# Kernel tuning notes

Measured on AMD Instinct MI355X. Metric: run time of the kernel, lower is better.

## Reference

```python
import jax, jax.numpy as jnp
import numpy as np

N_EMBEDS = 1024
N_HEADS = 16
EPS = 1e-3


def layer_norm(x, gamma, beta):
    mean = jnp.mean(x, axis=-1, keepdims=True)
    var = jnp.mean((x - mean) ** 2, axis=-1, keepdims=True)
    return gamma * (x - mean) / jnp.sqrt(var + EPS) + beta


def setup_inputs() -> dict:
    key = jax.random.key(0)
    ks = jax.random.split(key, 8)
    B, T, C = 4, 2048, N_EMBEDS
    s = 1.0 / np.sqrt(C)
    return {
        "x": jax.random.normal(ks[0], (B, T, C), dtype=jnp.float32),
        "w_qkv": jax.random.normal(ks[1], (C, 3 * C), dtype=jnp.float32) * s,
        "w_proj": jax.random.normal(ks[2], (C, C), dtype=jnp.float32) * s,
        "b_proj": jnp.zeros((C,), dtype=jnp.float32),
        "w1": jax.random.normal(ks[3], (C, 4 * C), dtype=jnp.float32) * s,
        "b1": jnp.zeros((4 * C,), dtype=jnp.float32),
        "w2": jax.random.normal(ks[4], (4 * C, C), dtype=jnp.float32) * (0.5 / np.sqrt(C)),
        "b2": jnp.zeros((C,), dtype=jnp.float32),
        "gamma1": jnp.ones((C,), dtype=jnp.float32),
        "beta1": jnp.zeros((C,), dtype=jnp.float32),
        "gamma2": jnp.ones((C,), dtype=jnp.float32),
        "beta2": jnp.zeros((C,), dtype=jnp.float32),
    }


def reference(x, w_qkv, w_proj, b_proj, w1, b1, w2, b2, gamma1, beta1, gamma2, beta2):
    B, T, C = x.shape
    H = N_HEADS
    D = C // H
    scale = D ** -0.5

    # --- attention sub-layer (pre-LN) ---
    h = layer_norm(x, gamma1, beta1)
    qkv = h @ w_qkv                      # [B,T,3C]
    q, k, v = jnp.split(qkv, 3, axis=-1)
    q = q.reshape(B, T, H, D).transpose(0, 2, 1, 3)  # [B,H,T,D]
    k = k.reshape(B, T, H, D).transpose(0, 2, 1, 3)
    v = v.reshape(B, T, H, D).transpose(0, 2, 1, 3)
    att = jnp.einsum('bhqd,bhkd->bhqk', q, k) * scale
    causal = jnp.tril(jnp.ones((T, T), dtype=bool))
    att = jnp.where(causal[None, None], att, jnp.float32(-1e9))
    att = jax.nn.softmax(att, axis=-1)
    out = jnp.einsum('bhqk,bhkd->bhqd', att, v)
    out = out.transpose(0, 2, 1, 3).reshape(B, T, C)
    x = x + out @ w_proj + b_proj

    # --- FFN sub-layer (pre-LN, erf-GELU) ---
    h = layer_norm(x, gamma2, beta2)
    h = jax.nn.gelu(h @ w1 + b1, approximate=False)
    x = x + h @ w2 + b2
    return x
```

## Files before the change

### kernel.cpp

```cpp
#include <hip/hip_runtime.h>
#include <hip/hip_bf16.h>
#include <cstdint>
#include <cstddef>

#define B_ 4
#define T_ 2048
#define C_ 1024
#define H_ 16
#define D_ 64
#define M_ (B_*T_)

using bf16_t = __hip_bfloat16;
typedef __bf16 v8bf __attribute__((ext_vector_type(8)));
typedef float  v4f  __attribute__((ext_vector_type(4)));
typedef float  f32x16 __attribute__((ext_vector_type(16)));

#define QSCALE (0.125f * 1.44269504088896340736f)

static __device__ __forceinline__ bf16_t f2bf(float v){ return __float2bfloat16(v); }

static __device__ __forceinline__ void glds16(const bf16_t* g, bf16_t* l){
  __builtin_amdgcn_global_load_lds((__attribute__((address_space(1))) void*)g,
                                   (__attribute__((address_space(3))) void*)l, 16, 0, 0);
}

static __device__ __forceinline__ uint32_t cvt_pk_bf16(float lo, float hi){
  uint32_t w;
  asm("v_cvt_pk_bf16_f32 %0, %1, %2" : "=v"(w) : "v"(lo), "v"(hi));
  return w;
}

__global__ void k_transpose_cast(const float* __restrict__ in, bf16_t* __restrict__ out,
                                 int K, int N){
  __shared__ float tile[32][33];
  int k0 = blockIdx.y*32, n0 = blockIdx.x*32;
  int tx = threadIdx.x, ty = threadIdx.y;
  #pragma unroll
  for(int j=0;j<32;j+=8) tile[ty+j][tx] = in[(size_t)(k0+ty+j)*N + n0+tx];
  __syncthreads();
  #pragma unroll
  for(int j=0;j<32;j+=8) out[(size_t)(n0+ty+j)*K + k0+tx] = f2bf(tile[tx][ty+j]);
}

__global__ __launch_bounds__(256) void k_layernorm(const float* __restrict__ x,
                                                   const float* __restrict__ gamma,
                                                   const float* __restrict__ beta,
                                                   bf16_t* __restrict__ out){
  int row = blockIdx.x;
  int tid = threadIdx.x;
  const float4 v = reinterpret_cast<const float4*>(x + (size_t)row*C_)[tid];
  float s  = v.x+v.y+v.z+v.w;
  float ss = v.x*v.x+v.y*v.y+v.z*v.z+v.w*v.w;
  #pragma unroll
  for(int m=1;m<64;m<<=1){ s += __shfl_xor(s,m); ss += __shfl_xor(ss,m); }
  __shared__ float sbuf[4], ssbuf[4];
  int wid = tid>>6, lane = tid&63;
  if(lane==0){ sbuf[wid]=s; ssbuf[wid]=ss; }
  __syncthreads();
  s  = sbuf[0]+sbuf[1]+sbuf[2]+sbuf[3];
  ss = ssbuf[0]+ssbuf[1]+ssbuf[2]+ssbuf[3];
  float mean = s * (1.0f/C_);
  float var  = ss * (1.0f/C_) - mean*mean;
  float rstd = rsqrtf(var + 1e-3f);
  const float4 g = reinterpret_cast<const float4*>(gamma)[tid];
  const float4 b = reinterpret_cast<const float4*>(beta)[tid];
  union { ushort4 u; bf16_t h[4]; } pk;
  pk.h[0] = f2bf(g.x*(v.x-mean)*rstd + b.x);
  pk.h[1] = f2bf(g.y*(v.y-mean)*rstd + b.y);
  pk.h[2] = f2bf(g.z*(v.z-mean)*rstd + b.z);
  pk.h[3] = f2bf(g.w*(v.w-mean)*rstd + b.w);
  *reinterpret_cast<ushort4*>(out + (size_t)row*C_ + tid*4) = pk.u;
}

template<int MODE>
__global__ __launch_bounds__(512, 4)
void k_gemm(const bf16_t* __restrict__ A, const bf16_t* __restrict__ Bt,
            const float* __restrict__ bias, const float* resid,
            void* out0, void* out1, void* out2,
            int N, int K, int gx)
{
  __shared__ __align__(16) bf16_t As[2][256*32];
  __shared__ __align__(16) bf16_t Bs[2][128*32];
  const int tid = threadIdx.x, lane = tid & 63, w = tid >> 6;
  const int wm = w >> 1, wn = w & 1;

  const int nwg = gx * 32;
  const int orig = blockIdx.y * gx + blockIdx.x;
  const int swz = (orig & 7) * (nwg >> 3) + (orig >> 3);
  const int ct = swz % gx, rt = swz / gx;
  const int row0 = rt * 256, col0 = ct * 128;

  const int sswz  = ((lane & 3) ^ ((lane >> 3) & 3)) * 8;
  const int srowA = w * 32 + (lane >> 2);
  const int srowB = w * 16 + (lane >> 2);
  const bf16_t* Ag = A  + (size_t)(row0 + srowA) * K + sswz;
  const bf16_t* Bg = Bt + (size_t)(col0 + srowB) * K + sswz;

  const int rdswz = (((lane >> 4) ^ (((lane & 15) >> 1) & 3))) * 8;

  v4f acc[4][4] = {};
  const int NT = K >> 5;

  auto stage = [&](int tt, int bb){
    const size_t ko = (size_t)tt * 32;
    glds16(Ag + ko,                 &As[bb][(w*32     )*32]);
    glds16(Ag + (size_t)16*K + ko,  &As[bb][(w*32 + 16)*32]);
    glds16(Bg + ko,                 &Bs[bb][(w*16     )*32]);
  };

  stage(0, 0);
  for (int t = 0; t < NT; ++t) {
    const int b = t & 1;
    if (t + 1 < NT) {
      stage(t + 1, b ^ 1);
      asm volatile("s_waitcnt vmcnt(3)" ::: "memory");
    } else {
      asm volatile("s_waitcnt vmcnt(0)" ::: "memory");
    }
    __builtin_amdgcn_s_barrier();
    __builtin_amdgcn_sched_barrier(0);
    const bf16_t* Ab = &As[b][0];
    const bf16_t* Bb = &Bs[b][0];
    v8bf af[4], bfv[4];
    #pragma unroll
    for (int m = 0; m < 4; ++m) {
      const int r = wm*64 + m*16 + (lane & 15);
      af[m] = *reinterpret_cast<const v8bf*>(Ab + r*32 + rdswz);
    }
    #pragma unroll
    for (int n = 0; n < 4; ++n) {
      const int r = wn*64 + n*16 + (lane & 15);
      bfv[n] = *reinterpret_cast<const v8bf*>(Bb + r*32 + rdswz);
    }
    __builtin_amdgcn_s_setprio(1);
    #pragma unroll
    for (int m = 0; m < 4; ++m)
      #pragma unroll
      for (int n = 0; n < 4; ++n)
        acc[m][n] = __builtin_amdgcn_mfma_f32_16x16x32_bf16(af[m], bfv[n], acc[m][n], 0,0,0);
    __builtin_amdgcn_s_setprio(0);
    __builtin_amdgcn_sched_barrier(0);
    __builtin_amdgcn_s_barrier();
  }

  #pragma unroll
  for (int mf = 0; mf < 4; ++mf) {
    const int rbase = row0 + wm*64 + mf*16 + (lane>>4)*4;
    #pragma unroll
    for (int nf = 0; nf < 4; ++nf) {
      const int c = col0 + wn*64 + nf*16 + (lane&15);
      #pragma unroll
      for (int i = 0; i < 4; ++i) {
        const int rr = rbase + i;
        float v = acc[mf][nf][i];
        if constexpr(MODE==0){
          const int sec = c >> 10, cc = c & 1023;
          const int h = cc >> 6, d = cc & 63;
          const int b = rr >> 11, t = rr & 2047;
          if(sec==0)      ((bf16_t*)out0)[((size_t)(b*H_ + h)*T_ + t)*D_ + d] = f2bf(v * QSCALE);
          else if(sec==1) ((bf16_t*)out1)[((size_t)(b*H_ + h)*T_ + t)*D_ + d] = f2bf(v);
          else            ((bf16_t*)out2)[((size_t)(b*H_ + h)*D_ + d)*T_ + t] = f2bf(v);
        } else if constexpr(MODE==1){
          ((float*)out0)[(size_t)rr*N + c] = v + bias[c] + resid[(size_t)rr*N + c];
        } else if constexpr(MODE==2){
          float o = v + bias[c];
          o = 0.5f*o*(1.0f + erff(o*0.70710678118f));
          ((bf16_t*)out0)[(size_t)rr*N + c] = f2bf(o);
        } else {
          ((float*)out0)[(size_t)rr*N + c] = v + bias[c] + resid[(size_t)rr*N + c];
        }
      }
    }
  }
}

__global__ __launch_bounds__(256)
void k_attn(const bf16_t* __restrict__ Q, const bf16_t* __restrict__ Kg,
            const bf16_t* __restrict__ Vt, bf16_t* __restrict__ O)
{
  __shared__ __align__(16) bf16_t Ks [64][72];
  __shared__ __align__(16) bf16_t Vts[64][72];
  __shared__ __align__(16) bf16_t Os [128][72];
  const int bh = blockIdx.y;
  const int pair = blockIdx.x;
  const int tid = threadIdx.x, lane = tid & 63, w = tid >> 6;
  const int ql = lane & 31, hi = lane >> 5;
  const int srow = tid >> 2;
  const int scol = (tid & 3) * 16;
  const bf16_t* Kgp = Kg + ((size_t)bh*T_ + srow)*D_ + scol;
  const bf16_t* Vtp = Vt + ((size_t)bh*D_ + srow)*T_ + scol;
  const int b = bh >> 4, h = bh & 15;

  for(int half=0; half<2; ++half){
    const int qt = half ? pair : (15 - pair);
    const int qbase = qt*128 + w*32;
    const int q = qbase + ql;

    v8bf qf[4];
    {
      const bf16_t* Qb = Q + ((size_t)bh*T_ + q)*D_ + hi*8;
      #pragma unroll
      for(int ds=0; ds<4; ds++)
        qf[ds] = *reinterpret_cast<const v8bf*>(Qb + ds*16);
    }

    f32x16 accO[2] = {};
    float mrun = -1e30f, lrun = 0.0f;
    const int NT = (qt + 1) * 2;

    v8bf kr0 = *reinterpret_cast<const v8bf*>(Kgp);
    v8bf kr1 = *reinterpret_cast<const v8bf*>(Kgp + 8);
    v8bf vr0 = *reinterpret_cast<const v8bf*>(Vtp);
    v8bf vr1 = *reinterpret_cast<const v8bf*>(Vtp + 8);

    for(int t=0; t<NT; t++){
      const int kv0 = t*64;
      *reinterpret_cast<v8bf*>(&Ks [srow][scol  ]) = kr0;
      *reinterpret_cast<v8bf*>(&Ks [srow][scol+8]) = kr1;
      *reinterpret_cast<v8bf*>(&Vts[srow][scol  ]) = vr0;
      *reinterpret_cast<v8bf*>(&Vts[srow][scol+8]) = vr1;
      __syncthreads();
      if(t+1 < NT){
        const size_t kn = (size_t)(kv0 + 64);
        kr0 = *reinterpret_cast<const v8bf*>(Kgp + kn*D_);
        kr1 = *reinterpret_cast<const v8bf*>(Kgp + kn*D_ + 8);
        vr0 = *reinterpret_cast<const v8bf*>(Vtp + kn);
        vr1 = *reinterpret_cast<const v8bf*>(Vtp + kn + 8);
      }

      if(kv0 <= qbase + 31){
        f32x16 sT[2] = {};
        #pragma unroll
        for(int kvh=0; kvh<2; kvh++)
          #pragma unroll
          for(int ds=0; ds<4; ds++){
            v8bf kf = *reinterpret_cast<const v8bf*>(&Ks[kvh*32 + ql][ds*16 + hi*8]);
            sT[kvh] = __builtin_amdgcn_mfma_f32_32x32x16_bf16(kf, qf[ds], sT[kvh], 0,0,0);
          }

        if(kv0 + 63 > qbase){
          const int qrel = q - kv0 - hi*4;
          #pragma unroll
          for(int kvh=0; kvh<2; kvh++)
            #pragma unroll
            for(int r=0; r<16; r++){
              const int c = kvh*32 + (r&3) + 8*(r>>2);
              if(c > qrel) sT[kvh][r] = -1e30f;
            }
        }

        float pm = sT[0][0];
        #pragma unroll
        for(int r=1; r<16; r++) pm = fmaxf(pm, sT[0][r]);
        #pragma unroll
        for(int r=0; r<16; r++) pm = fmaxf(pm, sT[1][r]);
        pm = fmaxf(pm, __shfl_xor(pm, 32));

        if(__any(pm - mrun > 8.0f)){
          const float mnew = fmaxf(mrun, pm);
          const float corr = __builtin_amdgcn_exp2f(mrun - mnew);
          mrun = mnew;
          lrun *= corr;
          #pragma unroll
          for(int dh=0; dh<2; dh++)
            #pragma unroll
            for(int r=0; r<16; r++) accO[dh][r] *= corr;
        }

        float rs = 0.0f;
        #pragma unroll
        for(int kvh=0; kvh<2; kvh++)
          #pragma unroll
          for(int r=0; r<16; r++){
            float p = __builtin_amdgcn_exp2f(sT[kvh][r] - mrun);
            sT[kvh][r] = p;
            rs += p;
          }
        rs += __shfl_xor(rs, 32);
        lrun += rs;

        v8bf pfrag[4];
        #pragma unroll
        for(int s4=0; s4<4; s4++){
          const int kvh = s4>>1, bb = (s4&1)*8;
          uint32_t wa = cvt_pk_bf16(sT[kvh][bb+0], sT[kvh][bb+1]);
          uint32_t wb = cvt_pk_bf16(sT[kvh][bb+2], sT[kvh][bb+3]);
          uint32_t wc = cvt_pk_bf16(sT[kvh][bb+4], sT[kvh][bb+5]);
          uint32_t wd = cvt_pk_bf16(sT[kvh][bb+6], sT[kvh][bb+7]);
          uint32_t xwa = (uint32_t)__shfl_xor((int)wa, 32);
          uint32_t xwb = (uint32_t)__shfl_xor((int)wb, 32);
          uint32_t xwc = (uint32_t)__shfl_xor((int)wc, 32);
          uint32_t xwd = (uint32_t)__shfl_xor((int)wd, 32);
          union { uint32_t u[4]; v8bf v; } pk;
          pk.u[0] = hi ? xwc : wa;
          pk.u[1] = hi ? xwd : wb;
          pk.u[2] = hi ? wc  : xwa;
          pk.u[3] = hi ? wd  : xwb;
          pfrag[s4] = pk.v;
        }

        #pragma unroll
        for(int dh=0; dh<2; dh++)
          #pragma unroll
          for(int s4=0; s4<4; s4++){
            v8bf vf = *reinterpret_cast<const v8bf*>(&Vts[dh*32 + ql][s4*16 + hi*8]);
            accO[dh] = __builtin_amdgcn_mfma_f32_32x32x16_bf16(vf, pfrag[s4], accO[dh], 0,0,0);
          }
      }
      __syncthreads();
    }

    const float inv = 1.0f / lrun;
    #pragma unroll
    for(int dh=0; dh<2; dh++)
      #pragma unroll
      for(int rg=0; rg<4; rg++){
        uint32_t lo_ = cvt_pk_bf16(accO[dh][rg*4+0]*inv, accO[dh][rg*4+1]*inv);
        uint32_t hi_ = cvt_pk_bf16(accO[dh][rg*4+2]*inv, accO[dh][rg*4+3]*inv);
        uint2 w2; w2.x = lo_; w2.y = hi_;
        *reinterpret_cast<uint2*>(&Os[w*32 + ql][dh*32 + rg*8 + hi*4]) = w2;
      }
    __syncthreads();
    const int orow = tid >> 1, ocol = (tid & 1) * 32;
    bf16_t* Og = O + ((size_t)(b*T_ + qt*128 + orow))*C_ + h*64 + ocol;
    #pragma unroll
    for(int j=0;j<4;j++)
      *reinterpret_cast<v8bf*>(Og + j*8) = *reinterpret_cast<const v8bf*>(&Os[orow][ocol + j*8]);
    __syncthreads();
  }
}

extern "C" void kernel_launch(void* const* d_in, const int* in_sizes, int n_in,
                              void* d_out, int out_size, void* d_ws, size_t ws_size,
                              hipStream_t stream) {
  const float* x      = (const float*)d_in[0];
  const float* w_qkv  = (const float*)d_in[1];
  const float* w_proj = (const float*)d_in[2];
  const float* b_proj = (const float*)d_in[3];
  const float* w1     = (const float*)d_in[4];
  const float* b1     = (const float*)d_in[5];
  const float* w2     = (const float*)d_in[6];
  const float* b2     = (const float*)d_in[7];
  const float* gamma1 = (const float*)d_in[8];
  const float* beta1  = (const float*)d_in[9];
  const float* gamma2 = (const float*)d_in[10];
  const float* beta2  = (const float*)d_in[11];

  char* ws = (char*)d_ws;
  bf16_t* wqkv_t  = (bf16_t*)(ws + 0);
  bf16_t* wproj_t = (bf16_t*)(ws + 6291456);
  bf16_t* w1_t    = (bf16_t*)(ws + 8388608);
  bf16_t* w2_t    = (bf16_t*)(ws + 16777216);
  bf16_t* qb      = (bf16_t*)(ws + 25165824);
  bf16_t* kb      = (bf16_t*)(ws + 41943040);
  bf16_t* vtb     = (bf16_t*)(ws + 58720256);
  bf16_t* obuf    = (bf16_t*)(ws + 75497472);
  bf16_t* hb      = (bf16_t*)(ws + 92274688);
  bf16_t* gb      = (bf16_t*)(ws + 25165824);
  float*  x2      = (float*)d_out;

  dim3 tb(32,8);
  k_transpose_cast<<<dim3(3072/32, 1024/32), tb, 0, stream>>>(w_qkv,  wqkv_t, 1024, 3072);
  k_transpose_cast<<<dim3(1024/32, 1024/32), tb, 0, stream>>>(w_proj, wproj_t,1024, 1024);
  k_transpose_cast<<<dim3(4096/32, 1024/32), tb, 0, stream>>>(w1,     w1_t,   1024, 4096);
  k_transpose_cast<<<dim3(1024/32, 4096/32), tb, 0, stream>>>(w2,     w2_t,   4096, 1024);

  k_layernorm<<<M_, 256, 0, stream>>>(x, gamma1, beta1, hb);

  k_gemm<0><<<dim3(24, 32), 512, 0, stream>>>(hb, wqkv_t, nullptr, nullptr,
                                              qb, kb, vtb, 3072, 1024, 24);
  k_attn<<<dim3(8, B_*H_), 256, 0, stream>>>(qb, kb, vtb, obuf);

  k_gemm<1><<<dim3(8, 32), 512, 0, stream>>>(obuf, wproj_t, b_proj, x,
                                             x2, nullptr, nullptr, 1024, 1024, 8);
  k_layernorm<<<M_, 256, 0, stream>>>(x2, gamma2, beta2, hb);

  k_gemm<2><<<dim3(32, 32), 512, 0, stream>>>(hb, w1_t, b1, nullptr,
                                              gb, nullptr, nullptr, 4096, 1024, 32);
  k_gemm<3><<<dim3(8, 32), 512, 0, stream>>>(gb, w2_t, b2, x2,
                                             d_out, nullptr, nullptr, 1024, 4096, 8);
}
```

Before: 438.8 us.

## Replace GEMM with 256x256 tile, 8-wave ping-pong pipelined kernel

Replaces the 256x128 K=32 double-buffered GEMM with a 256x256 tile, K=64 kernel in which each of the 8 waves computes a 128x64 sub-tile. Loads into LDS are interleaved with quarter-tile MFMA groups across barriers, so global loads overlap with compute. The LDS layout uses an 8-way XOR swizzle. The aim is more reuse per loaded byte and better latency hiding. The cost is one workgroup per CU, a large register footprint, and fewer workgroups for the N=1024 GEMMs (128 blocks, below the 256 CUs).

```diff
diff --git a/kernel.cpp b/kernel.cpp
--- a/kernel.cpp
+++ b/kernel.cpp
@@ -73,79 +73,122 @@
 }
 
 template<int MODE>
-__global__ __launch_bounds__(512, 4)
-void k_gemm(const bf16_t* __restrict__ A, const bf16_t* __restrict__ Bt,
-            const float* __restrict__ bias, const float* resid,
-            void* out0, void* out1, void* out2,
-            int N, int K, int gx)
+__global__ __launch_bounds__(512, 1)
+void k_gemm8(const bf16_t* __restrict__ A, const bf16_t* __restrict__ Bt,
+             const float* __restrict__ bias, const float* resid,
+             void* out0, void* out1, void* out2,
+             int N, int K, int gx)
 {
-  __shared__ __align__(16) bf16_t As[2][256*32];
-  __shared__ __align__(16) bf16_t Bs[2][128*32];
+  __shared__ __align__(16) bf16_t As[2][2][128*64];
+  __shared__ __align__(16) bf16_t Bs[2][2][128*64];
   const int tid = threadIdx.x, lane = tid & 63, w = tid >> 6;
-  const int wm = w >> 1, wn = w & 1;
+  const int wm = w >> 2, wn = w & 3;
 
   const int nwg = gx * 32;
   const int orig = blockIdx.y * gx + blockIdx.x;
   const int swz = (orig & 7) * (nwg >> 3) + (orig >> 3);
   const int ct = swz % gx, rt = swz / gx;
-  const int row0 = rt * 256, col0 = ct * 128;
-
-  const int sswz  = ((lane & 3) ^ ((lane >> 3) & 3)) * 8;
-  const int srowA = w * 32 + (lane >> 2);
-  const int srowB = w * 16 + (lane >> 2);
-  const bf16_t* Ag = A  + (size_t)(row0 + srowA) * K + sswz;
-  const bf16_t* Bg = Bt + (size_t)(col0 + srowB) * K + sswz;
-
-  const int rdswz = (((lane >> 4) ^ (((lane & 15) >> 1) & 3))) * 8;
-
-  v4f acc[4][4] = {};
-  const int NT = K >> 5;
-
-  auto stage = [&](int tt, int bb){
-    const size_t ko = (size_t)tt * 32;
-    glds16(Ag + ko,                 &As[bb][(w*32     )*32]);
-    glds16(Ag + (size_t)16*K + ko,  &As[bb][(w*32 + 16)*32]);
-    glds16(Bg + ko,                 &Bs[bb][(w*16     )*32]);
+  const int row0 = rt * 256, col0 = ct * 256;
+
+  const int sswz = ((lane & 7) ^ ((lane >> 3) & 7)) * 8;
+  const int srow = w * 8 + (lane >> 3);
+  const bf16_t* Agb = A  + (size_t)(row0 + srow) * K + sswz;
+  const bf16_t* Bgb = Bt + (size_t)(col0 + srow) * K + sswz;
+
+  auto stageA = [&](int tt, int hh){
+    const bf16_t* src = Agb + (size_t)(hh * 128) * K + tt * 64;
+    bf16_t* dst = &As[tt & 1][hh][w * 512];
+    glds16(src, dst);
+    glds16(src + (size_t)64 * K, dst + 4096);
   };
-
-  stage(0, 0);
-  for (int t = 0; t < NT; ++t) {
-    const int b = t & 1;
-    if (t + 1 < NT) {
-      stage(t + 1, b ^ 1);
-      asm volatile("s_waitcnt vmcnt(3)" ::: "memory");
-    } else {
-      asm volatile("s_waitcnt vmcnt(0)" ::: "memory");
-    }
-    __builtin_amdgcn_s_barrier();
-    __builtin_amdgcn_sched_barrier(0);
-    const bf16_t* Ab = &As[b][0];
-    const bf16_t* Bb = &Bs[b][0];
-    v8bf af[4], bfv[4];
-    #pragma unroll
-    for (int m = 0; m < 4; ++m) {
-      const int r = wm*64 + m*16 + (lane & 15);
-      af[m] = *reinterpret_cast<const v8bf*>(Ab + r*32 + rdswz);
-    }
-    #pragma unroll
-    for (int n = 0; n < 4; ++n) {
-      const int r = wn*64 + n*16 + (lane & 15);
-      bfv[n] = *reinterpret_cast<const v8bf*>(Bb + r*32 + rdswz);
-    }
-    __builtin_amdgcn_s_setprio(1);
+  auto stageB = [&](int tt, int hh){
+    const bf16_t* src = Bgb + (size_t)(hh * 128) * K + tt * 64;
+    bf16_t* dst = &Bs[tt & 1][hh][w * 512];
+    glds16(src, dst);
+    glds16(src + (size_t)64 * K, dst + 4096);
+  };
+
+  v8bf af[4][2], bfv[4][2];
+  v4f acc[8][4] = {};
+
+  auto LDA = [&](int bb, int mh){
+    const bf16_t* base = &As[bb][wm][0];
     #pragma unroll
     for (int m = 0; m < 4; ++m)
       #pragma unroll
-      for (int n = 0; n < 4; ++n)
-        acc[m][n] = __builtin_amdgcn_mfma_f32_16x16x32_bf16(af[m], bfv[n], acc[m][n], 0,0,0);
-    __builtin_amdgcn_s_setprio(0);
-    __builtin_amdgcn_sched_barrier(0);
-    __builtin_amdgcn_s_barrier();
+      for (int kk = 0; kk < 2; ++kk) {
+        const int r  = mh*64 + m*16 + (lane & 15);
+        const int sl = (kk*4 + (lane >> 4)) ^ (lane & 7);
+        af[m][kk] = *reinterpret_cast<const v8bf*>(base + r*64 + sl*8);
+      }
+  };
+  auto LDB = [&](int bb){
+    const bf16_t* base = &Bs[bb][wn >> 1][0];
+    #pragma unroll
+    for (int n = 0; n < 4; ++n)
+      #pragma unroll
+      for (int kk = 0; kk < 2; ++kk) {
+        const int r  = (wn & 1)*64 + n*16 + (lane & 15);
+        const int sl = (kk*4 + (lane >> 4)) ^ (lane & 7);
+        bfv[n][kk] = *reinterpret_cast<const v8bf*>(base + r*64 + sl*8);
+      }
+  };
+
+#define MFMA_Q(mh_, nh_) \
+  __builtin_amdgcn_s_setprio(1); \
+  _Pragma("unroll") \
+  for (int kk = 0; kk < 2; ++kk) \
+    _Pragma("unroll") \
+    for (int m = 0; m < 4; ++m) \
+      _Pragma("unroll") \
+      for (int n = 0; n < 2; ++n) \
+        acc[(mh_)*4+m][(nh_)*2+n] = __builtin_amdgcn_mfma_f32_16x16x32_bf16( \
+            af[m][kk], bfv[(nh_)*2+n][kk], acc[(mh_)*4+m][(nh_)*2+n], 0,0,0); \
+  __builtin_amdgcn_s_setprio(0);
+
+#define BAR()   __builtin_amdgcn_s_barrier()
+#define LGKM0() do { asm volatile("s_waitcnt lgkmcnt(0)" ::: "memory"); \
+                     __builtin_amdgcn_sched_barrier(0); } while(0)
+
+  stageA(0,0); stageA(0,1); stageB(0,0); stageB(0,1);
+  stageB(1,0); stageB(1,1); stageA(1,0);
+  asm volatile("s_waitcnt vmcnt(6)" ::: "memory");
+  BAR();
+
+  const int NP = (K >> 6) >> 1;
+  for (int j = 0; j < NP; ++j) {
+    const int t2 = 2*j + 2, t3 = 2*j + 3;
+    const bool more = (j + 1 < NP);
+    LDA(0, 0); LDB(0);
+    stageA(2*j + 1, 1);
+    BAR(); LGKM0(); MFMA_Q(0, 0); BAR();
+    if (more) stageB(t2, 0);
+    BAR(); MFMA_Q(0, 1); BAR();
+    LDA(0, 1);
+    if (more) stageB(t2, 1);
+    BAR(); LGKM0(); MFMA_Q(1, 0); BAR();
+    if (more) { stageA(t2, 0); asm volatile("s_waitcnt vmcnt(6)" ::: "memory"); }
+    else      {                asm volatile("s_waitcnt vmcnt(0)" ::: "memory"); }
+    BAR(); MFMA_Q(1, 1); BAR();
+    LDA(1, 0); LDB(1);
+    if (more) stageA(t2, 1);
+    BAR(); LGKM0(); MFMA_Q(0, 0); BAR();
+    if (more) stageB(t3, 0);
+    BAR(); MFMA_Q(0, 1); BAR();
+    LDA(1, 1);
+    if (more) stageB(t3, 1);
+    BAR(); LGKM0(); MFMA_Q(1, 0); BAR();
+    if (more) { stageA(t3, 0); asm volatile("s_waitcnt vmcnt(6)" ::: "memory"); }
+    else      {                asm volatile("s_waitcnt vmcnt(0)" ::: "memory"); }
+    BAR(); MFMA_Q(1, 1); BAR();
   }
+#undef MFMA_Q
+#undef BAR
+#undef LGKM0
 
   #pragma unroll
-  for (int mf = 0; mf < 4; ++mf) {
-    const int rbase = row0 + wm*64 + mf*16 + (lane>>4)*4;
+  for (int mf = 0; mf < 8; ++mf) {
+    const int rbase = row0 + wm*128 + mf*16 + (lane>>4)*4;
     #pragma unroll
     for (int nf = 0; nf < 4; ++nf) {
       const int c = col0 + wn*64 + nf*16 + (lane&15);
@@ -367,16 +410,16 @@
 
   k_layernorm<<<M_, 256, 0, stream>>>(x, gamma1, beta1, hb);
 
-  k_gemm<0><<<dim3(24, 32), 512, 0, stream>>>(hb, wqkv_t, nullptr, nullptr,
-                                              qb, kb, vtb, 3072, 1024, 24);
+  k_gemm8<0><<<dim3(12, 32), 512, 0, stream>>>(hb, wqkv_t, nullptr, nullptr,
+                                               qb, kb, vtb, 3072, 1024, 12);
   k_attn<<<dim3(8, B_*H_), 256, 0, stream>>>(qb, kb, vtb, obuf);
 
-  k_gemm<1><<<dim3(8, 32), 512, 0, stream>>>(obuf, wproj_t, b_proj, x,
-                                             x2, nullptr, nullptr, 1024, 1024, 8);
+  k_gemm8<1><<<dim3(4, 32), 512, 0, stream>>>(obuf, wproj_t, b_proj, x,
+                                              x2, nullptr, nullptr, 1024, 1024, 4);
   k_layernorm<<<M_, 256, 0, stream>>>(x2, gamma2, beta2, hb);
 
-  k_gemm<2><<<dim3(32, 32), 512, 0, stream>>>(hb, w1_t, b1, nullptr,
-                                              gb, nullptr, nullptr, 4096, 1024, 32);
-  k_gemm<3><<<dim3(8, 32), 512, 0, stream>>>(gb, w2_t, b2, x2,
-                                             d_out, nullptr, nullptr, 1024, 4096, 8);
-}
+  k_gemm8<2><<<dim3(16, 32), 512, 0, stream>>>(hb, w1_t, b1, nullptr,
+                                               gb, nullptr, nullptr, 4096, 1024, 16);
+  k_gemm8<3><<<dim3(4, 32), 512, 0, stream>>>(gb, w2_t, b2, x2,
+                                              d_out, nullptr, nullptr, 1024, 4096, 4);
+}
```

New measurement: 479.0 us. 9.2% more time.
